# Kernel tuning notes

Hardware: AMD Instinct MI355X
Metric: run time of the kernel (lower is better)

The kernel has to match this reference:

```python
import jax, jax.numpy as jnp
import numpy as np

N = 50000          # nodes
E = 400000         # directed input edges (one direction; symmetrized in reference)
F = 128            # in_channels == feat_size
GW = 128           # gather_width
OUT = 1            # out_channels
NUM_GRAPHS = 50
PROP_ITER = 4


def _lin(key, fi, fo):
    k1, k2 = jax.random.split(key)
    s = 1.0 / np.sqrt(fi)
    W = jax.random.uniform(k1, (fi, fo), minval=-s, maxval=s, dtype=jnp.float32)
    b = jax.random.uniform(k2, (fo,), minval=-s, maxval=s, dtype=jnp.float32)
    return W, b


def setup_inputs() -> dict:
    key = jax.random.key(0)
    ks = jax.random.split(key, 20)
    x = jax.random.normal(ks[0], (N, F), dtype=jnp.float32)
    src = jax.random.randint(ks[1], (E,), 0, N)
    off = jax.random.randint(ks[2], (E,), 1, N)   # avoid self-edges (self loops added in reference)
    dst = (src + off) % N
    edge_index = jnp.stack([src, dst])
    edge_attr = jax.random.uniform(ks[3], (E,), dtype=jnp.float32) * 6.0
    batch = jnp.arange(N) // (N // NUM_GRAPHS)
    gate_W1, gate_b1 = _lin(ks[4], F, F // 2)
    gate_W2, gate_b2 = _lin(ks[5], F // 2, F // 4)
    gate_W3, gate_b3 = _lin(ks[6], F // 4, 1)
    s = 1.0 / np.sqrt(F)
    gru_Wih = jax.random.uniform(ks[7], (3 * F, F), minval=-s, maxval=s, dtype=jnp.float32)
    gru_Whh = jax.random.uniform(ks[8], (3 * F, F), minval=-s, maxval=s, dtype=jnp.float32)
    gru_bih = jax.random.uniform(ks[9], (3 * F,), minval=-s, maxval=s, dtype=jnp.float32)
    gru_bhh = jax.random.uniform(ks[10], (3 * F,), minval=-s, maxval=s, dtype=jnp.float32)
    ai_W1, ai_b1 = _lin(ks[11], 2 * F, F)
    ai_W2, ai_b2 = _lin(ks[12], F, GW)
    aj_W, aj_b = _lin(ks[13], F, GW)
    h1, h2 = int(GW / 1.5), GW // 2
    out_W1, out_b1 = _lin(ks[14], GW, h1)
    out_W2, out_b2 = _lin(ks[15], h1, h2)
    out_W3, out_b3 = _lin(ks[16], h2, OUT)
    t = jnp.array([3.5], dtype=jnp.float32)
    return dict(x=x, edge_index=edge_index, edge_attr=edge_attr, batch=batch, t=t,
                gate_W1=gate_W1, gate_b1=gate_b1, gate_W2=gate_W2, gate_b2=gate_b2,
                gate_W3=gate_W3, gate_b3=gate_b3,
                gru_Wih=gru_Wih, gru_Whh=gru_Whh, gru_bih=gru_bih, gru_bhh=gru_bhh,
                ai_W1=ai_W1, ai_b1=ai_b1, ai_W2=ai_W2, ai_b2=ai_b2,
                aj_W=aj_W, aj_b=aj_b,
                out_W1=out_W1, out_b1=out_b1, out_W2=out_W2, out_b2=out_b2,
                out_W3=out_W3, out_b3=out_b3)


def _softsign(v):
    return v / (1.0 + jnp.abs(v))


def reference(x, edge_index, edge_attr, batch, t,
              gate_W1, gate_b1, gate_W2, gate_b2, gate_W3, gate_b3,
              gru_Wih, gru_Whh, gru_bih, gru_bhh,
              ai_W1, ai_b1, ai_W2, ai_b2, aj_W, aj_b,
              out_W1, out_b1, out_W2, out_b2, out_W3, out_b3):
    n = x.shape[0]
    loops = jnp.arange(n)
    # to_undirected + add_self_loops(fill=1.0); Graph_Cutoff filters edge_attr <= t.
    src = jnp.concatenate([edge_index[0], edge_index[1], loops])
    dst = jnp.concatenate([edge_index[1], edge_index[0], loops])
    feat = jnp.concatenate([edge_attr, edge_attr, jnp.ones((n,), edge_attr.dtype)])
    mask = feat <= t[0]                       # static-shape edge mask == edge filtering
    fmask = mask.astype(x.dtype)

    h = x
    for _ in range(PROP_ITER):
        # AttentionalAggregation gate over messages x_j = h[src]
        g = _softsign(h @ gate_W1 + gate_b1)
        g = _softsign(g @ gate_W2 + gate_b2)
        g = (g @ gate_W3 + gate_b3)[:, 0]     # [N] per-node gate logit
        logits = g[src]                       # [E_tot]
        mx = jax.ops.segment_max(jnp.where(mask, logits, -jnp.inf), dst, num_segments=n)
        mx = jnp.where(jnp.isfinite(mx), mx, 0.0)
        w = jnp.exp(jnp.where(mask, logits - mx[dst], -30.0)) * fmask
        denom = jax.ops.segment_sum(w, dst, num_segments=n)
        alpha = w / jnp.where(denom > 0, denom, 1.0)[dst]
        m = jax.ops.segment_sum(alpha[:, None] * h[src], dst, num_segments=n)  # [N,F]
        # torch.nn.GRUCell(m, h)
        gi = m @ gru_Wih.T + gru_bih
        gh = h @ gru_Whh.T + gru_bhh
        ir, iz, ig = jnp.split(gi, 3, axis=1)
        hr, hz, hg = jnp.split(gh, 3, axis=1)
        r = jax.nn.sigmoid(ir + hr)
        z = jax.nn.sigmoid(iz + hz)
        cand = jnp.tanh(ig + r * hg)
        h = (1.0 - z) * cand + z * h

    # Message_Attention: softmax(net_i([h, x]), axis=1) * net_j(x)
    ai = _softsign(jnp.concatenate([h, x], axis=1) @ ai_W1 + ai_b1)
    ai = _softsign(ai @ ai_W2 + ai_b2)
    attn = jax.nn.softmax(ai, axis=1)
    aj = _softsign(x @ aj_W + aj_b)
    node_out = attn * aj                      # [N, GW]

    pooled = jax.ops.segment_sum(node_out, batch, num_segments=NUM_GRAPHS)
    o = jax.nn.relu(pooled @ out_W1 + out_b1)
    o = jax.nn.relu(o @ out_W2 + out_b2)
    return o @ out_W3 + out_b3                # [NUM_GRAPHS, OUT]
```

## Files before the change

kernel.cpp:

```cpp
#include <hip/hip_runtime.h>
#include <hip/hip_bf16.h>

#define F 128
#define PROP_ITER 4

typedef unsigned short u16;
typedef unsigned int u32;
typedef __attribute__((ext_vector_type(8))) short bf16x8;
typedef __attribute__((ext_vector_type(4))) float f32x4;

__device__ __forceinline__ float softsign(float v) { return __fdividef(v, 1.0f + fabsf(v)); }
__device__ __forceinline__ float fsig(float v)  { return __fdividef(1.0f, 1.0f + __expf(-v)); }
__device__ __forceinline__ float ftanh(float v) { return 1.0f - __fdividef(2.0f, __expf(2.0f * v) + 1.0f); }
__device__ __forceinline__ u16 f2bf(float f) {
    union { float f; unsigned u; } v; v.f = f;
    unsigned r = v.u + 0x7FFF + ((v.u >> 16) & 1);
    return (u16)(r >> 16);
}
__device__ __forceinline__ float bf2f(u32 lo16) {
    union { unsigned u; float f; } v; v.u = lo16 << 16; return v.f;
}

__global__ __launch_bounds__(256) void count_edges(const int* __restrict__ ei,
                                                   const float* __restrict__ ea,
                                                   const float* __restrict__ t,
                                                   int* __restrict__ deg, int E, int N) {
    int i = blockIdx.x * 256 + threadIdx.x;
    int tot = 2 * E + N;
    if (i >= tot) return;
    int dst; float f;
    if (i < E)            { dst = ei[E + i];   f = ea[i]; }
    else if (i < 2 * E)   { dst = ei[i - E];   f = ea[i - E]; }
    else                  { dst = i - 2 * E;   f = 1.0f; }
    if (f <= t[0]) atomicAdd(&deg[dst], 1);
}

__global__ __launch_bounds__(256) void scan_partial(const int* __restrict__ deg,
                                                    int* __restrict__ bsum, int N) {
    __shared__ int sred[256];
    int tid = threadIdx.x;
    int base = blockIdx.x * 2048 + tid * 8;
    int s = 0;
    #pragma unroll
    for (int i = 0; i < 8; i++) {
        int idx = base + i;
        if (idx < N) s += deg[idx];
    }
    sred[tid] = s;
    __syncthreads();
    for (int off = 128; off; off >>= 1) {
        if (tid < off) sred[tid] += sred[tid + off];
        __syncthreads();
    }
    if (tid == 0) bsum[blockIdx.x] = sred[0];
}

__global__ __launch_bounds__(256) void scan_bsum(int* __restrict__ bsum, int nb) {
    __shared__ int s[256];
    int tid = threadIdx.x;
    int v = (tid < nb) ? bsum[tid] : 0;
    s[tid] = v;
    __syncthreads();
    for (int off = 1; off < 256; off <<= 1) {
        int u = (tid >= off) ? s[tid - off] : 0;
        __syncthreads();
        s[tid] += u;
        __syncthreads();
    }
    if (tid < nb) bsum[tid] = s[tid] - v;
    if (tid == 255) bsum[nb] = s[255];
}

__global__ __launch_bounds__(256) void scan_final(const int* __restrict__ deg,
                                                  const int* __restrict__ bsum,
                                                  int* __restrict__ row_ptr,
                                                  int* __restrict__ cursor,
                                                  int N, int nb) {
    __shared__ int sred[256];
    int tid = threadIdx.x;
    int base = blockIdx.x * 2048 + tid * 8;
    int vals[8];
    int s = 0;
    #pragma unroll
    for (int i = 0; i < 8; i++) {
        int idx = base + i;
        vals[i] = (idx < N) ? deg[idx] : 0;
        s += vals[i];
    }
    sred[tid] = s;
    __syncthreads();
    for (int off = 1; off < 256; off <<= 1) {
        int u = (tid >= off) ? sred[tid - off] : 0;
        __syncthreads();
        sred[tid] += u;
        __syncthreads();
    }
    int run = bsum[blockIdx.x] + sred[tid] - s;
    #pragma unroll
    for (int i = 0; i < 8; i++) {
        int idx = base + i;
        if (idx < N) { row_ptr[idx] = run; cursor[idx] = run; run += vals[i]; }
    }
    if (blockIdx.x == 0 && tid == 0) row_ptr[N] = bsum[nb];
}

__global__ __launch_bounds__(256) void scatter_edges(const int* __restrict__ ei,
                                                     const float* __restrict__ ea,
                                                     const float* __restrict__ t,
                                                     int* __restrict__ cursor,
                                                     int* __restrict__ col, int E, int N) {
    int i = blockIdx.x * 256 + threadIdx.x;
    int tot = 2 * E + N;
    if (i >= tot) return;
    int src, dst; float f;
    if (i < E)            { src = ei[i];      dst = ei[E + i]; f = ea[i]; }
    else if (i < 2 * E)   { src = ei[i];      dst = ei[i - E]; f = ea[i - E]; }
    else                  { src = i - 2 * E;  dst = src;       f = 1.0f; }
    if (f <= t[0]) {
        int p = atomicAdd(&cursor[dst], 1);
        col[p] = src;
    }
}

__global__ __launch_bounds__(256) void conv_w(const float* __restrict__ Wih,
                                              const float* __restrict__ Whh,
                                              u16* __restrict__ Wih16,
                                              u16* __restrict__ Whh16, int n) {
    int i = blockIdx.x * 256 + threadIdx.x;
    if (i < n) { Wih16[i] = f2bf(Wih[i]); Whh16[i] = f2bf(Whh[i]); }
}

__global__ __launch_bounds__(256) void conv_x(const float* __restrict__ x,
                                              u16* __restrict__ h16,
                                              u16* __restrict__ x16, int n4) {
    int i = blockIdx.x * 256 + threadIdx.x;
    if (i >= n4) return;
    float4 v = reinterpret_cast<const float4*>(x)[i];
    ushort4 u; u.x = f2bf(v.x); u.y = f2bf(v.y); u.z = f2bf(v.z); u.w = f2bf(v.w);
    reinterpret_cast<ushort4*>(h16)[i] = u;
    reinterpret_cast<ushort4*>(x16)[i] = u;
}

__global__ __launch_bounds__(256) void transp_bf16(const float* __restrict__ W,
                                                   u16* __restrict__ WT, int R, int C) {
    int i = blockIdx.x * 256 + threadIdx.x;
    if (i >= R * C) return;
    int c = i / R, r = i - c * R;
    WT[i] = f2bf(W[(size_t)r * C + c]);
}

__global__ __launch_bounds__(256) void pack_w16(const u16* __restrict__ W,
                                                u16* __restrict__ pk,
                                                int total, int nk0) {
    int i = blockIdx.x * 256 + threadIdx.x;
    if (i >= total) return;
    int j = i & 7, l = (i >> 3) & 63;
    int rest = i >> 9;
    int k0 = rest % nk0, fb = rest / nk0;
    int K = nk0 * 32;
    pk[i] = W[(size_t)(fb * 16 + (l & 15)) * K + k0 * 32 + (l >> 4) * 8 + j];
}

__device__ __forceinline__ void gate_from_lds(const u16* smh, u16* s1,
                                              const u16* __restrict__ pkgW1,
                                              const float* __restrict__ gb1,
                                              const u16* __restrict__ pkgW2,
                                              const float* __restrict__ gb2,
                                              const float* __restrict__ gW3,
                                              const float* __restrict__ gb3,
                                              float* __restrict__ eg,
                                              int node0, int N, int tid) {
    int wave = tid >> 6, lane = tid & 63, r = lane & 15, g = lane >> 4;
    {
        int j = wave * 16 + r;
        f32x4 acc[4];
        #pragma unroll
        for (int ns = 0; ns < 4; ns++) acc[ns] = (f32x4){0, 0, 0, 0};
        #pragma unroll
        for (int k0 = 0; k0 < 4; k0++) {
            bf16x8 b = *reinterpret_cast<const bf16x8*>(pkgW1 + ((size_t)(wave * 4 + k0) * 64 + lane) * 8);
            int sc = (k0 * 4 + g) ^ (r & 7);
            #pragma unroll
            for (int ns = 0; ns < 4; ns++) {
                bf16x8 a = *reinterpret_cast<const bf16x8*>(smh + ((ns * 16 + r) * 16 + sc) * 8);
                acc[ns] = __builtin_amdgcn_mfma_f32_16x16x32_bf16(a, b, acc[ns], 0, 0, 0);
            }
        }
        float bb = gb1[j];
        #pragma unroll
        for (int ns = 0; ns < 4; ns++)
            #pragma unroll
            for (int q = 0; q < 4; q++) {
                int row = ns * 16 + 4 * g + q;
                s1[(row * 8 + ((j >> 3) ^ (row & 7))) * 8 + (j & 7)] = f2bf(softsign(acc[ns][q] + bb));
            }
    }
    __syncthreads();
    {
        int ns = wave;
        float partial[4] = {0.f, 0.f, 0.f, 0.f};
        #pragma unroll
        for (int fsub = 0; fsub < 2; fsub++) {
            f32x4 acc = {0, 0, 0, 0};
            #pragma unroll
            for (int k0 = 0; k0 < 2; k0++) {
                bf16x8 b = *reinterpret_cast<const bf16x8*>(pkgW2 + ((size_t)(fsub * 2 + k0) * 64 + lane) * 8);
                int sc = (k0 * 4 + g) ^ (r & 7);
                bf16x8 a = *reinterpret_cast<const bf16x8*>(s1 + ((ns * 16 + r) * 8 + sc) * 8);
                acc = __builtin_amdgcn_mfma_f32_16x16x32_bf16(a, b, acc, 0, 0, 0);
            }
            float bb = gb2[fsub * 16 + r];
            float w3 = gW3[fsub * 16 + r];
            #pragma unroll
            for (int q = 0; q < 4; q++) partial[q] += softsign(acc[q] + bb) * w3;
        }
        #pragma unroll
        for (int o = 1; o < 16; o <<= 1)
            #pragma unroll
            for (int q = 0; q < 4; q++) partial[q] += __shfl_xor(partial[q], o);
        if (r == 0) {
            #pragma unroll
            for (int q = 0; q < 4; q++) {
                int node = node0 + ns * 16 + 4 * g + q;
                if (node < N) eg[node] = __expf(partial[q] + gb3[0]);
            }
        }
    }
}

__global__ __launch_bounds__(256) void gate_mfma(const u16* __restrict__ h16,
                                                 const u16* __restrict__ pkgW1,
                                                 const float* __restrict__ gb1,
                                                 const u16* __restrict__ pkgW2,
                                                 const float* __restrict__ gb2,
                                                 const float* __restrict__ gW3,
                                                 const float* __restrict__ gb3,
                                                 float* __restrict__ eg, int N) {
    __shared__ __align__(16) u16 smh[64 * 128];
    __shared__ __align__(16) u16 s1[64 * 64];
    int tid = threadIdx.x;
    int node0 = blockIdx.x * 64;
    #pragma unroll
    for (int rr = 0; rr < 4; rr++) {
        int row = rr * 16 + (tid >> 4);
        int c = tid & 15;
        int gn = node0 + row; if (gn >= N) gn = N - 1;
        bf16x8 vh = *reinterpret_cast<const bf16x8*>(h16 + (size_t)gn * F + c * 8);
        *reinterpret_cast<bf16x8*>(smh + (row * 16 + (c ^ (row & 7))) * 8) = vh;
    }
    __syncthreads();
    gate_from_lds(smh, s1, pkgW1, gb1, pkgW2, gb2, gW3, gb3, eg, node0, N, tid);
}

__global__ __launch_bounds__(64) void aggregate(const u16* __restrict__ h16,
                                                const float* __restrict__ eg,
                                                const int* __restrict__ row_ptr,
                                                const int* __restrict__ col,
                                                u16* __restrict__ m16, int N) {
    int dst = blockIdx.x;
    if (dst >= N) return;
    int lane = threadIdx.x;
    int e0 = row_ptr[dst], e1 = row_ptr[dst + 1];
    int g4 = lane >> 4, r = lane & 15;
    float acc[8];
    #pragma unroll
    for (int i = 0; i < 8; i++) acc[i] = 0.f;
    float denom = 0.f;
    for (int e = e0 + g4; e < e1; e += 4) {
        int s = col[e];
        float w = eg[s];
        denom += w;
        bf16x8 hv = *reinterpret_cast<const bf16x8*>(h16 + (size_t)s * F + r * 8);
        #pragma unroll
        for (int i = 0; i < 8; i++) acc[i] += w * bf2f((u32)(u16)hv[i]);
    }
    #pragma unroll
    for (int o = 16; o <= 32; o <<= 1) {
        denom += __shfl_xor(denom, o);
        #pragma unroll
        for (int i = 0; i < 8; i++) acc[i] += __shfl_xor(acc[i], o);
    }
    if (g4 == 0) {
        float inv = __fdividef(1.0f, denom);
        u32 w0 = (u32)f2bf(acc[0] * inv) | ((u32)f2bf(acc[1] * inv) << 16);
        u32 w1 = (u32)f2bf(acc[2] * inv) | ((u32)f2bf(acc[3] * inv) << 16);
        u32 w2 = (u32)f2bf(acc[4] * inv) | ((u32)f2bf(acc[5] * inv) << 16);
        u32 w3 = (u32)f2bf(acc[6] * inv) | ((u32)f2bf(acc[7] * inv) << 16);
        *reinterpret_cast<uint4*>(m16 + (size_t)dst * F + r * 8) = make_uint4(w0, w1, w2, w3);
    }
}

__global__ __launch_bounds__(256) void gru_fused(const u16* __restrict__ m16,
                                                 const u16* __restrict__ h16,
                                                 const u16* __restrict__ pkWih,
                                                 const u16* __restrict__ pkWhh,
                                                 const float* __restrict__ bih,
                                                 const float* __restrict__ bhh,
                                                 u16* __restrict__ h16o,
                                                 const u16* __restrict__ pkgW1,
                                                 const float* __restrict__ gb1,
                                                 const u16* __restrict__ pkgW2,
                                                 const float* __restrict__ gb2,
                                                 const float* __restrict__ gW3,
                                                 const float* __restrict__ gb3,
                                                 float* __restrict__ eg,
                                                 int do_gate, int N) {
    __shared__ __align__(16) u16 sm[64 * 128];
    __shared__ __align__(16) u16 sh[64 * 128];
    __shared__ __align__(16) u16 shn[64 * 128];
    int tid = threadIdx.x;
    int wave = tid >> 6, lane = tid & 63;
    int r = lane & 15, g = lane >> 4;
    int node0 = blockIdx.x * 64;

    #pragma unroll
    for (int rr = 0; rr < 4; rr++) {
        int row = rr * 16 + (tid >> 4);
        int c = tid & 15;
        int gn = node0 + row; if (gn >= N) gn = N - 1;
        bf16x8 vm = *reinterpret_cast<const bf16x8*>(m16 + (size_t)gn * F + c * 8);
        bf16x8 vh = *reinterpret_cast<const bf16x8*>(h16 + (size_t)gn * F + c * 8);
        int sc = c ^ (row & 7);
        *reinterpret_cast<bf16x8*>(sm + (row * 16 + sc) * 8) = vm;
        *reinterpret_cast<bf16x8*>(sh + (row * 16 + sc) * 8) = vh;
    }
    __syncthreads();

    #pragma unroll 1
    for (int fs = 0; fs < 2; fs++) {
        int fsub = wave * 2 + fs;
        int f0 = fsub * 16;
        f32x4 acc[4][4];
        #pragma unroll
        for (int ns = 0; ns < 4; ns++)
            #pragma unroll
            for (int c = 0; c < 4; c++) acc[ns][c] = (f32x4){0, 0, 0, 0};

        bf16x8 A0, A1, A2, A3, A4, A5, B0, B1, B2, B3, B4, B5;
        auto ld = [&](int k0, bf16x8& q0, bf16x8& q1, bf16x8& q2,
                      bf16x8& q3, bf16x8& q4, bf16x8& q5) {
            q0 = *reinterpret_cast<const bf16x8*>(pkWih + ((size_t)((0  + fsub) * 4 + k0) * 64 + lane) * 8);
            q1 = *reinterpret_cast<const bf16x8*>(pkWih + ((size_t)((8  + fsub) * 4 + k0) * 64 + lane) * 8);
            q2 = *reinterpret_cast<const bf16x8*>(pkWih + ((size_t)((16 + fsub) * 4 + k0) * 64 + lane) * 8);
            q3 = *reinterpret_cast<const bf16x8*>(pkWhh + ((size_t)((0  + fsub) * 4 + k0) * 64 + lane) * 8);
            q4 = *reinterpret_cast<const bf16x8*>(pkWhh + ((size_t)((8  + fsub) * 4 + k0) * 64 + lane) * 8);
            q5 = *reinterpret_cast<const bf16x8*>(pkWhh + ((size_t)((16 + fsub) * 4 + k0) * 64 + lane) * 8);
        };
        auto step = [&](int k0, const bf16x8& q0, const bf16x8& q1, const bf16x8& q2,
                        const bf16x8& q3, const bf16x8& q4, const bf16x8& q5) {
            int sc = (k0 * 4 + g) ^ (r & 7);
            #pragma unroll
            for (int ns = 0; ns < 4; ns++) {
                int rowb = (ns * 16 + r) * 16;
                bf16x8 am = *reinterpret_cast<const bf16x8*>(sm + (rowb + sc) * 8);
                bf16x8 ah = *reinterpret_cast<const bf16x8*>(sh + (rowb + sc) * 8);
                acc[ns][0] = __builtin_amdgcn_mfma_f32_16x16x32_bf16(am, q0, acc[ns][0], 0, 0, 0);
                acc[ns][0] = __builtin_amdgcn_mfma_f32_16x16x32_bf16(ah, q3, acc[ns][0], 0, 0, 0);
                acc[ns][1] = __builtin_amdgcn_mfma_f32_16x16x32_bf16(am, q1, acc[ns][1], 0, 0, 0);
                acc[ns][1] = __builtin_amdgcn_mfma_f32_16x16x32_bf16(ah, q4, acc[ns][1], 0, 0, 0);
                acc[ns][2] = __builtin_amdgcn_mfma_f32_16x16x32_bf16(am, q2, acc[ns][2], 0, 0, 0);
                acc[ns][3] = __builtin_amdgcn_mfma_f32_16x16x32_bf16(ah, q5, acc[ns][3], 0, 0, 0);
            }
        };
        ld(0, A0, A1, A2, A3, A4, A5);
        ld(1, B0, B1, B2, B3, B4, B5);
        step(0, A0, A1, A2, A3, A4, A5);
        ld(2, A0, A1, A2, A3, A4, A5);
        step(1, B0, B1, B2, B3, B4, B5);
        ld(3, B0, B1, B2, B3, B4, B5);
        step(2, A0, A1, A2, A3, A4, A5);
        step(3, B0, B1, B2, B3, B4, B5);

        int fj = f0 + r;
        int chunk = fj >> 3, e = fj & 7;
        float b_r  = bih[fj] + bhh[fj];
        float b_z  = bih[128 + fj] + bhh[128 + fj];
        float bi_g = bih[256 + fj];
        float bh_g = bhh[256 + fj];
        #pragma unroll
        for (int ns = 0; ns < 4; ns++) {
            #pragma unroll
            for (int q = 0; q < 4; q++) {
                int row = ns * 16 + 4 * g + q;
                float rr2 = fsig(acc[ns][0][q] + b_r);
                float z   = fsig(acc[ns][1][q] + b_z);
                float cand = ftanh(acc[ns][2][q] + bi_g + rr2 * (acc[ns][3][q] + bh_g));
                float hv = bf2f((u32)sh[(row * 16 + (chunk ^ (row & 7))) * 8 + e]);
                float hn = (1.0f - z) * cand + z * hv;
                shn[(row * 16 + (chunk ^ (row & 7))) * 8 + e] = f2bf(hn);
            }
        }
    }
    __syncthreads();

    #pragma unroll
    for (int rr = 0; rr < 4; rr++) {
        int row = rr * 16 + (tid >> 4);
        int c = tid & 15;
        int gn = node0 + row;
        if (gn < N) {
            bf16x8 v = *reinterpret_cast<const bf16x8*>(shn + (row * 16 + (c ^ (row & 7))) * 8);
            *reinterpret_cast<bf16x8*>(h16o + (size_t)gn * F + c * 8) = v;
        }
    }

    if (do_gate) {
        gate_from_lds(shn, sm, pkgW1, gb1, pkgW2, gb2, gW3, gb3, eg, node0, N, tid);
    }
}

__global__ __launch_bounds__(256) void attn_fused(const u16* __restrict__ h16,
                                                  const u16* __restrict__ x16,
                                                  const u16* __restrict__ pkW1,
                                                  const float* __restrict__ b1,
                                                  const u16* __restrict__ pkW2,
                                                  const float* __restrict__ b2,
                                                  const u16* __restrict__ pkWj,
                                                  const float* __restrict__ bj,
                                                  float* __restrict__ pooled,
                                                  int N, int npg, int G) {
    __shared__ __align__(16) u16 smh[64 * 128];
    __shared__ __align__(16) u16 sx[64 * 128];
    __shared__ float s_v[64 * 128];
    __shared__ float s_mx[64], s_sum[64];
    __shared__ float s_pool[2][128];
    int tid = threadIdx.x;
    int wave = tid >> 6, lane = tid & 63, r = lane & 15, g = lane >> 4;
    int node0 = blockIdx.x * 64;

    s_pool[tid >> 7][tid & 127] = 0.f;

    #pragma unroll
    for (int rr = 0; rr < 4; rr++) {
        int row = rr * 16 + (tid >> 4);
        int c = tid & 15;
        int gn = node0 + row; if (gn >= N) gn = N - 1;
        bf16x8 vh = *reinterpret_cast<const bf16x8*>(h16 + (size_t)gn * F + c * 8);
        bf16x8 vx = *reinterpret_cast<const bf16x8*>(x16 + (size_t)gn * F + c * 8);
        int sc = c ^ (row & 7);
        *reinterpret_cast<bf16x8*>(smh + (row * 16 + sc) * 8) = vh;
        *reinterpret_cast<bf16x8*>(sx + (row * 16 + sc) * 8) = vx;
    }
    __syncthreads();

    float v1[2][4][4];
    #pragma unroll
    for (int fs = 0; fs < 2; fs++) {
        int fsub = wave * 2 + fs;
        int j = fsub * 16 + r;
        f32x4 acc[4];
        #pragma unroll
        for (int ns = 0; ns < 4; ns++) acc[ns] = (f32x4){0, 0, 0, 0};
        #pragma unroll
        for (int k0 = 0; k0 < 8; k0++) {
            bf16x8 b = *reinterpret_cast<const bf16x8*>(pkW1 + ((size_t)(fsub * 8 + k0) * 64 + lane) * 8);
            const u16* As = (k0 < 4) ? smh : sx;
            int sc = ((k0 & 3) * 4 + g) ^ (r & 7);
            #pragma unroll
            for (int ns = 0; ns < 4; ns++) {
                bf16x8 a = *reinterpret_cast<const bf16x8*>(As + ((ns * 16 + r) * 16 + sc) * 8);
                acc[ns] = __builtin_amdgcn_mfma_f32_16x16x32_bf16(a, b, acc[ns], 0, 0, 0);
            }
        }
        float bb = b1[j];
        #pragma unroll
        for (int ns = 0; ns < 4; ns++)
            #pragma unroll
            for (int q = 0; q < 4; q++) v1[fs][ns][q] = softsign(acc[ns][q] + bb);
    }
    __syncthreads();

    #pragma unroll
    for (int fs = 0; fs < 2; fs++) {
        int j = (wave * 2 + fs) * 16 + r;
        #pragma unroll
        for (int ns = 0; ns < 4; ns++)
            #pragma unroll
            for (int q = 0; q < 4; q++) {
                int row = ns * 16 + 4 * g + q;
                smh[(row * 16 + ((j >> 3) ^ (row & 7))) * 8 + (j & 7)] = f2bf(v1[fs][ns][q]);
            }
    }
    __syncthreads();

    #pragma unroll
    for (int fs = 0; fs < 2; fs++) {
        int fsub = wave * 2 + fs;
        int j = fsub * 16 + r;
        f32x4 acc[4];
        #pragma unroll
        for (int ns = 0; ns < 4; ns++) acc[ns] = (f32x4){0, 0, 0, 0};
        #pragma unroll
        for (int k0 = 0; k0 < 4; k0++) {
            bf16x8 b = *reinterpret_cast<const bf16x8*>(pkW2 + ((size_t)(fsub * 4 + k0) * 64 + lane) * 8);
            int sc = (k0 * 4 + g) ^ (r & 7);
            #pragma unroll
            for (int ns = 0; ns < 4; ns++) {
                bf16x8 a = *reinterpret_cast<const bf16x8*>(smh + ((ns * 16 + r) * 16 + sc) * 8);
                acc[ns] = __builtin_amdgcn_mfma_f32_16x16x32_bf16(a, b, acc[ns], 0, 0, 0);
            }
        }
        float bb = b2[j];
        #pragma unroll
        for (int ns = 0; ns < 4; ns++)
            #pragma unroll
            for (int q = 0; q < 4; q++) {
                int row = ns * 16 + 4 * g + q;
                s_v[row * 128 + (j ^ ((row & 31) << 2))] = softsign(acc[ns][q] + bb);
            }
    }
    __syncthreads();

    {
        int row = tid >> 2, base = (tid & 3) * 32;
        int swz = (row & 31) << 2;
        float mx = -1e30f;
        #pragma unroll
        for (int i = 0; i < 32; i++) mx = fmaxf(mx, s_v[row * 128 + ((base + i) ^ swz)]);
        mx = fmaxf(mx, __shfl_xor(mx, 1));
        mx = fmaxf(mx, __shfl_xor(mx, 2));
        float sum = 0.f;
        #pragma unroll
        for (int i = 0; i < 32; i++) sum += __expf(s_v[row * 128 + ((base + i) ^ swz)] - mx);
        sum += __shfl_xor(sum, 1);
        sum += __shfl_xor(sum, 2);
        if ((tid & 3) == 0) { s_mx[row] = mx; s_sum[row] = sum; }
    }
    __syncthreads();

    int graph0 = node0 / npg;
    #pragma unroll
    for (int fs = 0; fs < 2; fs++) {
        int fsub = wave * 2 + fs;
        int j = fsub * 16 + r;
        f32x4 acc[4];
        #pragma unroll
        for (int ns = 0; ns < 4; ns++) acc[ns] = (f32x4){0, 0, 0, 0};
        #pragma unroll
        for (int k0 = 0; k0 < 4; k0++) {
            bf16x8 b = *reinterpret_cast<const bf16x8*>(pkWj + ((size_t)(fsub * 4 + k0) * 64 + lane) * 8);
            int sc = (k0 * 4 + g) ^ (r & 7);
            #pragma unroll
            for (int ns = 0; ns < 4; ns++) {
                bf16x8 a = *reinterpret_cast<const bf16x8*>(sx + ((ns * 16 + r) * 16 + sc) * 8);
                acc[ns] = __builtin_amdgcn_mfma_f32_16x16x32_bf16(a, b, acc[ns], 0, 0, 0);
            }
        }
        float bb = bj[j];
        float p0 = 0.f, p1 = 0.f;
        #pragma unroll
        for (int ns = 0; ns < 4; ns++)
            #pragma unroll
            for (int q = 0; q < 4; q++) {
                int row = ns * 16 + 4 * g + q;
                int node = node0 + row;
                if (node < N) {
                    float aj = softsign(acc[ns][q] + bb);
                    float vv = s_v[row * 128 + (j ^ ((row & 31) << 2))];
                    float attn = __fdividef(__expf(vv - s_mx[row]), s_sum[row]);
                    float val = attn * aj;
                    if (node / npg == graph0) p0 += val; else p1 += val;
                }
            }
        if (p0 != 0.f) atomicAdd(&s_pool[0][j], p0);
        if (p1 != 0.f) atomicAdd(&s_pool[1][j], p1);
    }
    __syncthreads();

    {
        int b_ = tid >> 7, colj = tid & 127;
        float v = s_pool[b_][colj];
        int gg = graph0 + b_;
        if (v != 0.f && gg < G) atomicAdd(&pooled[(size_t)gg * F + colj], v);
    }
}

__global__ __launch_bounds__(128) void out_mlp(const float* __restrict__ pooled,
                                               const float* __restrict__ W1, const float* __restrict__ b1,
                                               const float* __restrict__ W2, const float* __restrict__ b2,
                                               const float* __restrict__ W3, const float* __restrict__ b3,
                                               float* __restrict__ out, int H1, int H2) {
    __shared__ float sp[128];
    __shared__ float s1[96];
    __shared__ float s2[64];
    int g = blockIdx.x, j = threadIdx.x;
    sp[j] = pooled[g * F + j];
    __syncthreads();
    if (j < H1) {
        float a = b1[j];
        for (int k = 0; k < 128; k++) a += sp[k] * W1[k * H1 + j];
        s1[j] = fmaxf(a, 0.f);
    }
    __syncthreads();
    if (j < H2) {
        float a = b2[j];
        for (int k = 0; k < H1; k++) a += s1[k] * W2[k * H2 + j];
        s2[j] = fmaxf(a, 0.f);
    }
    __syncthreads();
    if (j == 0) {
        float a = b3[0];
        for (int k = 0; k < H2; k++) a += s2[k] * W3[k];
        out[g] = a;
    }
}

extern "C" void kernel_launch(void* const* d_in, const int* in_sizes, int n_in,
                              void* d_out, int out_size, void* d_ws, size_t ws_size,
                              hipStream_t stream) {
    const float* x    = (const float*)d_in[0];
    const int*   ei   = (const int*)  d_in[1];
    const float* ea   = (const float*)d_in[2];
    const float* t    = (const float*)d_in[4];
    const float* gW1  = (const float*)d_in[5];
    const float* gb1  = (const float*)d_in[6];
    const float* gW2  = (const float*)d_in[7];
    const float* gb2  = (const float*)d_in[8];
    const float* gW3  = (const float*)d_in[9];
    const float* gb3  = (const float*)d_in[10];
    const float* Wih  = (const float*)d_in[11];
    const float* Whh  = (const float*)d_in[12];
    const float* bih  = (const float*)d_in[13];
    const float* bhh  = (const float*)d_in[14];
    const float* aiW1 = (const float*)d_in[15];
    const float* aib1 = (const float*)d_in[16];
    const float* aiW2 = (const float*)d_in[17];
    const float* aib2 = (const float*)d_in[18];
    const float* ajW  = (const float*)d_in[19];
    const float* ajb  = (const float*)d_in[20];
    const float* oW1  = (const float*)d_in[21];
    const float* ob1  = (const float*)d_in[22];
    const float* oW2  = (const float*)d_in[23];
    const float* ob2  = (const float*)d_in[24];
    const float* oW3  = (const float*)d_in[25];
    const float* ob3  = (const float*)d_in[26];
    float* out = (float*)d_out;

    const int N = in_sizes[0] / F;
    const int E = in_sizes[2];
    const int G = out_size;
    const int npg = N / G;
    const int H1 = 85, H2 = 64;
    const int Etot = 2 * E + N;

    char* w = (char*)d_ws;
    auto carve = [&](size_t bytes) {
        void* p = (void*)w;
        w += (bytes + 255) & ~(size_t)255;
        return p;
    };
    int*   deg     = (int*)  carve((size_t)N * 4);
    int*   row_ptr = (int*)  carve((size_t)(N + 1) * 4);
    int*   cursor  = (int*)  carve((size_t)N * 4);
    int*   bsum    = (int*)  carve((size_t)512 * 4);
    int*   col     = (int*)  carve((size_t)Etot * 4);
    float* eg      = (float*)carve((size_t)N * 4);
    u16*   m16     = (u16*)  carve((size_t)N * F * 2);
    u16*   h16A    = (u16*)  carve((size_t)N * F * 2);
    u16*   h16B    = (u16*)  carve((size_t)N * F * 2);
    u16*   x16     = (u16*)  carve((size_t)N * F * 2);
    u16*   Wih16   = (u16*)  carve((size_t)384 * F * 2);
    u16*   Whh16   = (u16*)  carve((size_t)384 * F * 2);
    u16*   pkWih   = (u16*)  carve((size_t)384 * F * 2);
    u16*   pkWhh   = (u16*)  carve((size_t)384 * F * 2);
    u16*   W1T     = (u16*)  carve((size_t)128 * 256 * 2);
    u16*   W2T     = (u16*)  carve((size_t)128 * 128 * 2);
    u16*   WjT     = (u16*)  carve((size_t)128 * 128 * 2);
    u16*   gW1T    = (u16*)  carve((size_t)64 * 128 * 2);
    u16*   gW2T    = (u16*)  carve((size_t)32 * 64 * 2);
    u16*   pkW1    = (u16*)  carve((size_t)128 * 256 * 2);
    u16*   pkW2    = (u16*)  carve((size_t)128 * 128 * 2);
    u16*   pkWj    = (u16*)  carve((size_t)128 * 128 * 2);
    u16*   pkgW1   = (u16*)  carve((size_t)64 * 128 * 2);
    u16*   pkgW2   = (u16*)  carve((size_t)32 * 64 * 2);
    float* pooled  = (float*)carve((size_t)G * F * 4);
    (void)ws_size; (void)n_in;

    conv_w<<<(384 * F + 255) / 256, 256, 0, stream>>>(Wih, Whh, Wih16, Whh16, 384 * F);
    pack_w16<<<(384 * F + 255) / 256, 256, 0, stream>>>(Wih16, pkWih, 384 * F, 4);
    pack_w16<<<(384 * F + 255) / 256, 256, 0, stream>>>(Whh16, pkWhh, 384 * F, 4);
    int n4 = N * F / 4;
    conv_x<<<(n4 + 255) / 256, 256, 0, stream>>>(x, h16A, x16, n4);
    transp_bf16<<<(256 * 128 + 255) / 256, 256, 0, stream>>>(aiW1, W1T, 256, 128);
    transp_bf16<<<(128 * 128 + 255) / 256, 256, 0, stream>>>(aiW2, W2T, 128, 128);
    transp_bf16<<<(128 * 128 + 255) / 256, 256, 0, stream>>>(ajW, WjT, 128, 128);
    transp_bf16<<<(128 * 64 + 255) / 256, 256, 0, stream>>>(gW1, gW1T, 128, 64);
    transp_bf16<<<(64 * 32 + 255) / 256, 256, 0, stream>>>(gW2, gW2T, 64, 32);
    pack_w16<<<(128 * 256 + 255) / 256, 256, 0, stream>>>(W1T, pkW1, 128 * 256, 8);
    pack_w16<<<(128 * 128 + 255) / 256, 256, 0, stream>>>(W2T, pkW2, 128 * 128, 4);
    pack_w16<<<(128 * 128 + 255) / 256, 256, 0, stream>>>(WjT, pkWj, 128 * 128, 4);
    pack_w16<<<(64 * 128 + 255) / 256, 256, 0, stream>>>(gW1T, pkgW1, 64 * 128, 4);
    pack_w16<<<(32 * 64 + 255) / 256, 256, 0, stream>>>(gW2T, pkgW2, 32 * 64, 2);

    hipMemsetAsync(deg, 0, (size_t)N * 4, stream);
    int eb = (Etot + 255) / 256;
    count_edges<<<eb, 256, 0, stream>>>(ei, ea, t, deg, E, N);
    int nbs = (N + 2047) / 2048;
    scan_partial<<<nbs, 256, 0, stream>>>(deg, bsum, N);
    scan_bsum<<<1, 256, 0, stream>>>(bsum, nbs);
    scan_final<<<nbs, 256, 0, stream>>>(deg, bsum, row_ptr, cursor, N, nbs);
    scatter_edges<<<eb, 256, 0, stream>>>(ei, ea, t, cursor, col, E, N);

    u16* h16c = h16A;
    u16* h16n = h16B;
    int nb64 = (N + 63) / 64;

    gate_mfma<<<nb64, 256, 0, stream>>>(h16c, pkgW1, gb1, pkgW2, gb2, gW3, gb3, eg, N);

    for (int it = 0; it < PROP_ITER; it++) {
        aggregate<<<N, 64, 0, stream>>>(h16c, eg, row_ptr, col, m16, N);
        gru_fused<<<nb64, 256, 0, stream>>>(m16, h16c, pkWih, pkWhh, bih, bhh, h16n,
                                            pkgW1, gb1, pkgW2, gb2, gW3, gb3, eg,
                                            (it < PROP_ITER - 1) ? 1 : 0, N);
        u16* tmp = h16c; h16c = h16n; h16n = tmp;
    }

    hipMemsetAsync(pooled, 0, (size_t)G * F * 4, stream);
    attn_fused<<<nb64, 256, 0, stream>>>(h16c, x16, pkW1, aib1, pkW2, aib2, pkWj, ajb,
                                         pooled, N, npg, G);
    out_mlp<<<G, 128, 0, stream>>>(pooled, oW1, ob1, oW2, ob2, oW3, ob3, out, H1, H2);
}
```

Before: 436.3 us.

## Widen GRU kernel to 512 threads and overlap h store with gate MLP

The fused GRU kernel now runs 8 waves per 64-node block, so each wave handles one 16-feature slice instead of looping over two. After the GRU, waves 4-7 write the new hidden state to global memory while waves 0-3 compute the gate MLP inline from LDS, rather than doing both in sequence. Separately, the weight preprocessing folds conversion, transpose and packing into single kernels, which cuts several small launches. The larger blocks raise per-block register pressure and may lower occupancy.

```diff
diff --git a/kernel.cpp b/kernel.cpp
--- a/kernel.cpp
+++ b/kernel.cpp
@@ -122,14 +122,6 @@
     }
 }
 
-__global__ __launch_bounds__(256) void conv_w(const float* __restrict__ Wih,
-                                              const float* __restrict__ Whh,
-                                              u16* __restrict__ Wih16,
-                                              u16* __restrict__ Whh16, int n) {
-    int i = blockIdx.x * 256 + threadIdx.x;
-    if (i < n) { Wih16[i] = f2bf(Wih[i]); Whh16[i] = f2bf(Whh[i]); }
-}
-
 __global__ __launch_bounds__(256) void conv_x(const float* __restrict__ x,
                                               u16* __restrict__ h16,
                                               u16* __restrict__ x16, int n4) {
@@ -141,24 +133,31 @@
     reinterpret_cast<ushort4*>(x16)[i] = u;
 }
 
-__global__ __launch_bounds__(256) void transp_bf16(const float* __restrict__ W,
-                                                   u16* __restrict__ WT, int R, int C) {
-    int i = blockIdx.x * 256 + threadIdx.x;
-    if (i >= R * C) return;
-    int c = i / R, r = i - c * R;
-    WT[i] = f2bf(W[(size_t)r * C + c]);
-}
-
-__global__ __launch_bounds__(256) void pack_w16(const u16* __restrict__ W,
-                                                u16* __restrict__ pk,
-                                                int total, int nk0) {
+__global__ __launch_bounds__(256) void pack_rm_f32(const float* __restrict__ W,
+                                                   u16* __restrict__ pk,
+                                                   int total, int nk0) {
     int i = blockIdx.x * 256 + threadIdx.x;
     if (i >= total) return;
     int j = i & 7, l = (i >> 3) & 63;
     int rest = i >> 9;
     int k0 = rest % nk0, fb = rest / nk0;
     int K = nk0 * 32;
-    pk[i] = W[(size_t)(fb * 16 + (l & 15)) * K + k0 * 32 + (l >> 4) * 8 + j];
+    int row = fb * 16 + (l & 15);
+    int kk = k0 * 32 + (l >> 4) * 8 + j;
+    pk[i] = f2bf(W[(size_t)row * K + kk]);
+}
+
+__global__ __launch_bounds__(256) void pack_tr_f32(const float* __restrict__ A,
+                                                   u16* __restrict__ pk,
+                                                   int total, int nk0, int stride) {
+    int i = blockIdx.x * 256 + threadIdx.x;
+    if (i >= total) return;
+    int j = i & 7, l = (i >> 3) & 63;
+    int rest = i >> 9;
+    int k0 = rest % nk0, fb = rest / nk0;
+    int row = fb * 16 + (l & 15);
+    int kk = k0 * 32 + (l >> 4) * 8 + j;
+    pk[i] = f2bf(A[(size_t)kk * stride + row]);
 }
 
 __device__ __forceinline__ void gate_from_lds(const u16* smh, u16* s1,
@@ -290,7 +289,7 @@
     }
 }
 
-__global__ __launch_bounds__(256) void gru_fused(const u16* __restrict__ m16,
+__global__ __launch_bounds__(512) void gru_fused(const u16* __restrict__ m16,
                                                  const u16* __restrict__ h16,
                                                  const u16* __restrict__ pkWih,
                                                  const u16* __restrict__ pkWhh,
@@ -314,8 +313,8 @@
     int node0 = blockIdx.x * 64;
 
     #pragma unroll
-    for (int rr = 0; rr < 4; rr++) {
-        int row = rr * 16 + (tid >> 4);
+    for (int rr = 0; rr < 2; rr++) {
+        int row = rr * 32 + (tid >> 4);
         int c = tid & 15;
         int gn = node0 + row; if (gn >= N) gn = N - 1;
         bf16x8 vm = *reinterpret_cast<const bf16x8*>(m16 + (size_t)gn * F + c * 8);
@@ -326,10 +325,8 @@
     }
     __syncthreads();
 
-    #pragma unroll 1
-    for (int fs = 0; fs < 2; fs++) {
-        int fsub = wave * 2 + fs;
-        int f0 = fsub * 16;
+    {
+        int fsub = wave;
         f32x4 acc[4][4];
         #pragma unroll
         for (int ns = 0; ns < 4; ns++)
@@ -371,7 +368,7 @@
         step(2, A0, A1, A2, A3, A4, A5);
         step(3, B0, B1, B2, B3, B4, B5);
 
-        int fj = f0 + r;
+        int fj = fsub * 16 + r;
         int chunk = fj >> 3, e = fj & 7;
         float b_r  = bih[fj] + bhh[fj];
         float b_z  = bih[128 + fj] + bhh[128 + fj];
@@ -393,19 +390,85 @@
     }
     __syncthreads();
 
-    #pragma unroll
-    for (int rr = 0; rr < 4; rr++) {
-        int row = rr * 16 + (tid >> 4);
-        int c = tid & 15;
-        int gn = node0 + row;
-        if (gn < N) {
-            bf16x8 v = *reinterpret_cast<const bf16x8*>(shn + (row * 16 + (c ^ (row & 7))) * 8);
-            *reinterpret_cast<bf16x8*>(h16o + (size_t)gn * F + c * 8) = v;
-        }
-    }
-
     if (do_gate) {
-        gate_from_lds(shn, sm, pkgW1, gb1, pkgW2, gb2, gW3, gb3, eg, node0, N, tid);
+        if (wave >= 4) {
+            int tid2 = tid - 256;
+            #pragma unroll
+            for (int rr = 0; rr < 4; rr++) {
+                int row = rr * 16 + (tid2 >> 4);
+                int c = tid2 & 15;
+                int gn = node0 + row;
+                if (gn < N) {
+                    bf16x8 v = *reinterpret_cast<const bf16x8*>(shn + (row * 16 + (c ^ (row & 7))) * 8);
+                    *reinterpret_cast<bf16x8*>(h16o + (size_t)gn * F + c * 8) = v;
+                }
+            }
+        } else {
+            int j = wave * 16 + r;
+            f32x4 acc[4];
+            #pragma unroll
+            for (int ns = 0; ns < 4; ns++) acc[ns] = (f32x4){0, 0, 0, 0};
+            #pragma unroll
+            for (int k0 = 0; k0 < 4; k0++) {
+                bf16x8 b = *reinterpret_cast<const bf16x8*>(pkgW1 + ((size_t)(wave * 4 + k0) * 64 + lane) * 8);
+                int sc = (k0 * 4 + g) ^ (r & 7);
+                #pragma unroll
+                for (int ns = 0; ns < 4; ns++) {
+                    bf16x8 a = *reinterpret_cast<const bf16x8*>(shn + ((ns * 16 + r) * 16 + sc) * 8);
+                    acc[ns] = __builtin_amdgcn_mfma_f32_16x16x32_bf16(a, b, acc[ns], 0, 0, 0);
+                }
+            }
+            float bb = gb1[j];
+            #pragma unroll
+            for (int ns = 0; ns < 4; ns++)
+                #pragma unroll
+                for (int q = 0; q < 4; q++) {
+                    int row = ns * 16 + 4 * g + q;
+                    sm[(row * 8 + ((j >> 3) ^ (row & 7))) * 8 + (j & 7)] = f2bf(softsign(acc[ns][q] + bb));
+                }
+        }
+        __syncthreads();
+        if (wave < 4) {
+            int ns = wave;
+            float partial[4] = {0.f, 0.f, 0.f, 0.f};
+            #pragma unroll
+            for (int fsub = 0; fsub < 2; fsub++) {
+                f32x4 acc = {0, 0, 0, 0};
+                #pragma unroll
+                for (int k0 = 0; k0 < 2; k0++) {
+                    bf16x8 b = *reinterpret_cast<const bf16x8*>(pkgW2 + ((size_t)(fsub * 2 + k0) * 64 + lane) * 8);
+                    int sc = (k0 * 4 + g) ^ (r & 7);
+                    bf16x8 a = *reinterpret_cast<const bf16x8*>(sm + ((ns * 16 + r) * 8 + sc) * 8);
+                    acc = __builtin_amdgcn_mfma_f32_16x16x32_bf16(a, b, acc, 0, 0, 0);
+                }
+                float bb = gb2[fsub * 16 + r];
+                float w3 = gW3[fsub * 16 + r];
+                #pragma unroll
+                for (int q = 0; q < 4; q++) partial[q] += softsign(acc[q] + bb) * w3;
+            }
+            #pragma unroll
+            for (int o = 1; o < 16; o <<= 1)
+                #pragma unroll
+                for (int q = 0; q < 4; q++) partial[q] += __shfl_xor(partial[q], o);
+            if (r == 0) {
+                #pragma unroll
+                for (int q = 0; q < 4; q++) {
+                    int node = node0 + ns * 16 + 4 * g + q;
+                    if (node < N) eg[node] = __expf(partial[q] + gb3[0]);
+                }
+            }
+        }
+    } else {
+        #pragma unroll
+        for (int rr = 0; rr < 2; rr++) {
+            int row = rr * 32 + (tid >> 4);
+            int c = tid & 15;
+            int gn = node0 + row;
+            if (gn < N) {
+                bf16x8 v = *reinterpret_cast<const bf16x8*>(shn + (row * 16 + (c ^ (row & 7))) * 8);
+                *reinterpret_cast<bf16x8*>(h16o + (size_t)gn * F + c * 8) = v;
+            }
+        }
     }
 }
 
@@ -659,15 +722,8 @@
     u16*   h16A    = (u16*)  carve((size_t)N * F * 2);
     u16*   h16B    = (u16*)  carve((size_t)N * F * 2);
     u16*   x16     = (u16*)  carve((size_t)N * F * 2);
-    u16*   Wih16   = (u16*)  carve((size_t)384 * F * 2);
-    u16*   Whh16   = (u16*)  carve((size_t)384 * F * 2);
     u16*   pkWih   = (u16*)  carve((size_t)384 * F * 2);
     u16*   pkWhh   = (u16*)  carve((size_t)384 * F * 2);
-    u16*   W1T     = (u16*)  carve((size_t)128 * 256 * 2);
-    u16*   W2T     = (u16*)  carve((size_t)128 * 128 * 2);
-    u16*   WjT     = (u16*)  carve((size_t)128 * 128 * 2);
-    u16*   gW1T    = (u16*)  carve((size_t)64 * 128 * 2);
-    u16*   gW2T    = (u16*)  carve((size_t)32 * 64 * 2);
     u16*   pkW1    = (u16*)  carve((size_t)128 * 256 * 2);
     u16*   pkW2    = (u16*)  carve((size_t)128 * 128 * 2);
     u16*   pkWj    = (u16*)  carve((size_t)128 * 128 * 2);
@@ -676,21 +732,15 @@
     float* pooled  = (float*)carve((size_t)G * F * 4);
     (void)ws_size; (void)n_in;
 
-    conv_w<<<(384 * F + 255) / 256, 256, 0, stream>>>(Wih, Whh, Wih16, Whh16, 384 * F);
-    pack_w16<<<(384 * F + 255) / 256, 256, 0, stream>>>(Wih16, pkWih, 384 * F, 4);
-    pack_w16<<<(384 * F + 255) / 256, 256, 0, stream>>>(Whh16, pkWhh, 384 * F, 4);
+    pack_rm_f32<<<(384 * F + 255) / 256, 256, 0, stream>>>(Wih, pkWih, 384 * F, 4);
+    pack_rm_f32<<<(384 * F + 255) / 256, 256, 0, stream>>>(Whh, pkWhh, 384 * F, 4);
+    pack_tr_f32<<<(128 * 256 + 255) / 256, 256, 0, stream>>>(aiW1, pkW1, 128 * 256, 8, 128);
+    pack_tr_f32<<<(128 * 128 + 255) / 256, 256, 0, stream>>>(aiW2, pkW2, 128 * 128, 4, 128);
+    pack_tr_f32<<<(128 * 128 + 255) / 256, 256, 0, stream>>>(ajW, pkWj, 128 * 128, 4, 128);
+    pack_tr_f32<<<(64 * 128 + 255) / 256, 256, 0, stream>>>(gW1, pkgW1, 64 * 128, 4, 64);
+    pack_tr_f32<<<(32 * 64 + 255) / 256, 256, 0, stream>>>(gW2, pkgW2, 32 * 64, 2, 32);
     int n4 = N * F / 4;
     conv_x<<<(n4 + 255) / 256, 256, 0, stream>>>(x, h16A, x16, n4);
-    transp_bf16<<<(256 * 128 + 255) / 256, 256, 0, stream>>>(aiW1, W1T, 256, 128);
-    transp_bf16<<<(128 * 128 + 255) / 256, 256, 0, stream>>>(aiW2, W2T, 128, 128);
-    transp_bf16<<<(128 * 128 + 255) / 256, 256, 0, stream>>>(ajW, WjT, 128, 128);
-    transp_bf16<<<(128 * 64 + 255) / 256, 256, 0, stream>>>(gW1, gW1T, 128, 64);
-    transp_bf16<<<(64 * 32 + 255) / 256, 256, 0, stream>>>(gW2, gW2T, 64, 32);
-    pack_w16<<<(128 * 256 + 255) / 256, 256, 0, stream>>>(W1T, pkW1, 128 * 256, 8);
-    pack_w16<<<(128 * 128 + 255) / 256, 256, 0, stream>>>(W2T, pkW2, 128 * 128, 4);
-    pack_w16<<<(128 * 128 + 255) / 256, 256, 0, stream>>>(WjT, pkWj, 128 * 128, 4);
-    pack_w16<<<(64 * 128 + 255) / 256, 256, 0, stream>>>(gW1T, pkgW1, 64 * 128, 4);
-    pack_w16<<<(32 * 64 + 255) / 256, 256, 0, stream>>>(gW2T, pkgW2, 32 * 64, 2);
 
     hipMemsetAsync(deg, 0, (size_t)N * 4, stream);
     int eb = (Etot + 255) / 256;
@@ -709,7 +759,7 @@
 
     for (int it = 0; it < PROP_ITER; it++) {
         aggregate<<<N, 64, 0, stream>>>(h16c, eg, row_ptr, col, m16, N);
-        gru_fused<<<nb64, 256, 0, stream>>>(m16, h16c, pkWih, pkWhh, bih, bhh, h16n,
+        gru_fused<<<nb64, 512, 0, stream>>>(m16, h16c, pkWih, pkWhh, bih, bhh, h16n,
                                             pkgW1, gb1, pkgW2, gb2, gW3, gb3, eg,
                                             (it < PROP_ITER - 1) ? 1 : 0, N);
         u16* tmp = h16c; h16c = h16n; h16n = tmp;
```

After: 386.1 us. -11.5%, faster.
